# Kernel tuning notes

Measured on AMD Instinct MI355X. Metric: run time of the kernel, lower is better.

The kernel has to match this reference:

```python
import jax, jax.numpy as jnp
import numpy as np

# Dims chosen per init_kwargs / input_specs
LEVELS = 2      # data_in_levels (residual binarization depth)
K = 4           # data_in_k (LUT fan-in)
KK = 2 ** K     # LUT table size
IN = 128        # in_features
OUT = 128       # out_features
BATCH = 128
T = IN * OUT    # tables_count = mask_builder.get_tables_count() * out_features


def setup_inputs() -> dict:
    key = jax.random.key(0)
    k1, k2, k3, k4 = jax.random.split(key, 4)
    x = jax.random.normal(k1, (BATCH, IN), dtype=jnp.float32)
    # trainer weight: one 2^k-entry LUT per table
    weight = jax.random.normal(k2, (T, KK), dtype=jnp.float32) * 0.1
    bias = jax.random.normal(k3, (OUT,), dtype=jnp.float32) * 0.1
    # means init: ars = levels..1 (reversed arange+1), normalized
    ars = (np.arange(LEVELS) + 1.0)[::-1]
    means = jnp.asarray(ars / ars.sum(), dtype=jnp.float32)
    # MaskExpanded: per (out_feature, in_feature) table of k input indices;
    # first index is the table's own in_idx, the rest drawn from the others.
    rnd = jax.random.randint(k4, (OUT, IN, K), 0, IN)
    first = jnp.broadcast_to(jnp.arange(IN)[None, :, None], (OUT, IN, 1))
    input_mask = jnp.concatenate([first, rnd[..., 1:]], axis=-1).reshape(-1).astype(jnp.int32)
    return {"x": x, "weight": weight, "bias": bias, "means": means, "input_mask": input_mask}


def _truth_table():
    # all 2^k bipolar codes in {-1,+1}^k, shape [KK, K]
    codes = (jnp.arange(KK)[:, None] >> jnp.arange(K)[None, :]) & 1
    return (2 * codes - 1).astype(jnp.float32)


def residual_sign(x, means):
    # ReBNet residual sign quantizer: level-l output is +-|means[l]|, residual updated
    resid = x
    outs = []
    for l in range(LEVELS):
        s = jnp.where(resid >= 0, 1.0, -1.0)  # bipolar binary_quantizer
        o = jnp.abs(means[l]) * s
        outs.append(o)
        resid = resid - o
    return jnp.stack(outs)  # [LEVELS, B, IN]


def reference(x, weight, bias, means, input_mask):
    B = x.shape[0]
    out_bin = residual_sign(x, means)                   # [L, B, IN]
    expanded = out_bin[:, :, input_mask]                # irregular gather -> [L, B, T*K]
    xk = expanded.reshape(LEVELS, B, T, K)              # per-table k inputs
    tt = _truth_table()                                 # [KK, K]
    # Lagrange basis on {-1,+1}^k: prod_i (1 + x_i * c_i) / 2  -> [L, B, T, KK]
    basis = jnp.prod((1.0 + xk[..., None, :] * tt) * 0.5, axis=-1)
    # LUT eval (contract KK) and sum over residual levels -> [B, T]
    table_out = jnp.einsum('lbtc,tc->bt', basis, weight)
    # grouped segment-sum: each output feature sums its in_features tables
    out = table_out.reshape(B, OUT, IN).sum(-1) + bias  # [B, OUT]
    return out
```

## Files before the change

### kernel.cpp

```cpp
#include <hip/hip_runtime.h>
#include <stdint.h>

#define IN_   128
#define OUT_  128
#define BATCH_ 128
#define KK_   16
#define BPB   32

__global__ __launch_bounds__(256) void linlut_kernel(
    const float* __restrict__ x, const float* __restrict__ w,
    const float* __restrict__ bias, const float* __restrict__ means,
    const int* __restrict__ mask, float* __restrict__ out)
{
    __shared__ float    lut[128 * 33];
    __shared__ uint32_t sbw[BPB * 33];
    __shared__ uint32_t pidx[128];

    const int tid = threadIdx.x;
    const int o  = blockIdx.x >> 2;
    const int b0 = (blockIdx.x & 3) * BPB;

    const float m0 = fabsf(means[0]);
    const float m1 = fabsf(means[1]);

    if (tid < 128) {
        const int4 mm = *(const int4*)(mask + ((size_t)(o * IN_ + tid)) * 4);
        pidx[tid] = (uint32_t)mm.x | ((uint32_t)mm.y << 8) |
                    ((uint32_t)mm.z << 16) | ((uint32_t)mm.w << 24);
    }

    #pragma unroll
    for (int r = 0; r < 4; ++r) {
        const int item = tid + 256 * r;
        const int b    = item >> 5;
        const int g    = item & 31;
        const float4 xv = *(const float4*)(x + (size_t)(b0 + b) * IN_ + g * 4);
        float vv[4] = {xv.x, xv.y, xv.z, xv.w};
        uint32_t wd = 0;
        #pragma unroll
        for (int k = 0; k < 4; ++k) {
            const uint32_t s0 = (vv[k] >= 0.0f) ? 1u : 0u;
            const float rr = vv[k] - (s0 ? m0 : -m0);
            const uint32_t s1 = (rr >= 0.0f) ? 1u : 0u;
            wd |= (s0 | (s1 << 1)) << (8 * k);
        }
        sbw[b * 33 + g] = wd;
    }

    {
        const int i   = tid >> 1;
        const int lvl = tid & 1;
        const float m = lvl ? m1 : m0;
        const float p = (1.0f + m) * 0.5f;
        const float q = (1.0f - m) * 0.5f;
        float pw[5];
        pw[0] = p * p * p * p;
        pw[1] = p * p * p * q;
        pw[2] = p * p * q * q;
        pw[3] = p * q * q * q;
        pw[4] = q * q * q * q;
        const float* wr = w + ((size_t)(o * IN_ + i)) * KK_;
        float wv[16];
        #pragma unroll
        for (int c4 = 0; c4 < 4; ++c4) {
            const float4 t = *(const float4*)(wr + 4 * c4);
            wv[4 * c4 + 0] = t.x; wv[4 * c4 + 1] = t.y;
            wv[4 * c4 + 2] = t.z; wv[4 * c4 + 3] = t.w;
        }
        float* lr = lut + i * 33 + lvl * 16;
        #pragma unroll
        for (int S = 0; S < 16; ++S) {
            float acc = 0.0f;
            #pragma unroll
            for (int c = 0; c < 16; ++c)
                acc += wv[c] * pw[__popc(S ^ c)];
            lr[S] = acc;
        }
    }
    __syncthreads();

    const int part = tid & 7;
    const int bloc = tid >> 3;
    const unsigned char* sbb = ((const unsigned char*)sbw) + bloc * 132;
    float acc = 0.0f;
    #pragma unroll
    for (int j = 0; j < 16; ++j) {
        const int i = part + 8 * j;
        const uint32_t pk = pidx[i];
        const uint32_t c0 = sbb[pk & 255u];
        const uint32_t c1 = sbb[(pk >> 8) & 255u];
        const uint32_t c2 = sbb[(pk >> 16) & 255u];
        const uint32_t c3 = sbb[pk >> 24];
        const uint32_t S0 = (c0 & 1u) | ((c1 & 1u) << 1) | ((c2 & 1u) << 2) | ((c3 & 1u) << 3);
        const uint32_t S1 = (c0 >> 1) | ((c1 >> 1) << 1) | ((c2 >> 1) << 2) | ((c3 >> 1) << 3);
        const float* lr = lut + i * 33;
        acc += lr[S0];
        acc += lr[16 + S1];
    }
    acc += __shfl_xor(acc, 1);
    acc += __shfl_xor(acc, 2);
    acc += __shfl_xor(acc, 4);
    if (part == 0) {
        const int b = b0 + bloc;
        out[(size_t)b * OUT_ + o] = acc + bias[o];
    }
}

extern "C" void kernel_launch(void* const* d_in, const int* in_sizes, int n_in,
                              void* d_out, int out_size, void* d_ws, size_t ws_size,
                              hipStream_t stream) {
    const float* x     = (const float*)d_in[0];
    const float* w     = (const float*)d_in[1];
    const float* bias  = (const float*)d_in[2];
    const float* means = (const float*)d_in[3];
    const int*   mask  = (const int*)d_in[4];
    float* out = (float*)d_out;
    hipLaunchKernelGGL(linlut_kernel, dim3(512), dim3(256), 0, stream,
                       x, w, bias, means, mask, out);
}
```

Measured before the change: 66.38 us.

## Transpose binarized input to feature-major bytes and reduce partials through shared memory

Stores the two-level sign bits as one byte per (feature, batch) in a transposed shared array, so the 32 lanes sharing a table read consecutive bytes of one feature row. Each lane now owns a batch column and loops over a contiguous range of tables, so the LUT read address is uniform across the lane group and becomes a broadcast rather than a scattered access. The shuffle reduction is replaced by a shared-memory partial array, an extra barrier, and a final sum over eight partials done by 32 threads. This trades cheaper, lower-conflict inner-loop LDS traffic for byte-granular stores during binarization and an extra synchronization.

Result: no change. 65.91 us (-0.7%).

```diff
diff --git a/kernel.cpp b/kernel.cpp
--- a/kernel.cpp
+++ b/kernel.cpp
@@ -1,20 +1,22 @@
 #include <hip/hip_runtime.h>
 #include <stdint.h>
 
-#define IN_   128
-#define OUT_  128
+#define IN_    128
+#define OUT_   128
 #define BATCH_ 128
-#define KK_   16
-#define BPB   32
+#define KK_    16
+#define BPB    32
+#define SBSTRIDE 36
 
 __global__ __launch_bounds__(256) void linlut_kernel(
     const float* __restrict__ x, const float* __restrict__ w,
     const float* __restrict__ bias, const float* __restrict__ means,
     const int* __restrict__ mask, float* __restrict__ out)
 {
-    __shared__ float    lut[128 * 33];
-    __shared__ uint32_t sbw[BPB * 33];
-    __shared__ uint32_t pidx[128];
+    __shared__ float         lut[128 * 33];
+    __shared__ unsigned char sbT[IN_ * SBSTRIDE];
+    __shared__ uint32_t      pidx[128];
+    __shared__ float         partial[8 * 33];
 
     const int tid = threadIdx.x;
     const int o  = blockIdx.x >> 2;
@@ -22,6 +24,7 @@
 
     const float m0 = fabsf(means[0]);
     const float m1 = fabsf(means[1]);
+    const float bo = bias[o];
 
     if (tid < 128) {
         const int4 mm = *(const int4*)(mask + ((size_t)(o * IN_ + tid)) * 4);
@@ -35,16 +38,14 @@
         const int b    = item >> 5;
         const int g    = item & 31;
         const float4 xv = *(const float4*)(x + (size_t)(b0 + b) * IN_ + g * 4);
-        float vv[4] = {xv.x, xv.y, xv.z, xv.w};
-        uint32_t wd = 0;
+        const float vv[4] = {xv.x, xv.y, xv.z, xv.w};
         #pragma unroll
         for (int k = 0; k < 4; ++k) {
             const uint32_t s0 = (vv[k] >= 0.0f) ? 1u : 0u;
             const float rr = vv[k] - (s0 ? m0 : -m0);
             const uint32_t s1 = (rr >= 0.0f) ? 1u : 0u;
-            wd |= (s0 | (s1 << 1)) << (8 * k);
+            sbT[(4 * g + k) * SBSTRIDE + b] = (unsigned char)(s0 | (s1 << 1));
         }
-        sbw[b * 33 + g] = wd;
     }
 
     {
@@ -79,30 +80,33 @@
     }
     __syncthreads();
 
-    const int part = tid & 7;
-    const int bloc = tid >> 3;
-    const unsigned char* sbb = ((const unsigned char*)sbw) + bloc * 132;
+    const int bcol = tid & 31;
+    const int part = tid >> 5;
+    const unsigned char* sb = sbT + bcol;
     float acc = 0.0f;
     #pragma unroll
     for (int j = 0; j < 16; ++j) {
-        const int i = part + 8 * j;
+        const int i = part * 16 + j;
         const uint32_t pk = pidx[i];
-        const uint32_t c0 = sbb[pk & 255u];
-        const uint32_t c1 = sbb[(pk >> 8) & 255u];
-        const uint32_t c2 = sbb[(pk >> 16) & 255u];
-        const uint32_t c3 = sbb[pk >> 24];
+        const uint32_t c0 = sb[(pk & 255u) * SBSTRIDE];
+        const uint32_t c1 = sb[((pk >> 8) & 255u) * SBSTRIDE];
+        const uint32_t c2 = sb[((pk >> 16) & 255u) * SBSTRIDE];
+        const uint32_t c3 = sb[(pk >> 24) * SBSTRIDE];
         const uint32_t S0 = (c0 & 1u) | ((c1 & 1u) << 1) | ((c2 & 1u) << 2) | ((c3 & 1u) << 3);
         const uint32_t S1 = (c0 >> 1) | ((c1 >> 1) << 1) | ((c2 >> 1) << 2) | ((c3 >> 1) << 3);
         const float* lr = lut + i * 33;
         acc += lr[S0];
         acc += lr[16 + S1];
     }
-    acc += __shfl_xor(acc, 1);
-    acc += __shfl_xor(acc, 2);
-    acc += __shfl_xor(acc, 4);
-    if (part == 0) {
-        const int b = b0 + bloc;
-        out[(size_t)b * OUT_ + o] = acc + bias[o];
+    partial[part * 33 + bcol] = acc;
+    __syncthreads();
+
+    if (tid < 32) {
+        float s = 0.0f;
+        #pragma unroll
+        for (int p = 0; p < 8; ++p)
+            s += partial[p * 33 + tid];
+        out[(size_t)(b0 + tid) * OUT_ + o] = s + bo;
     }
 }
 
```
